# Kernel tuning notes

Hardware: AMD Instinct MI355X
Metric: run time of the kernel (lower is better)

The kernel has to match this reference:

```python
import jax, jax.numpy as jnp
import numpy as np

IN_CH = 256
OUT_CH = 256
LATENT = 512
SCALE = 1.0 / IN_CH ** 0.5


def setup_inputs() -> dict:
    key = jax.random.key(0)
    k1, k2, k3, k4 = jax.random.split(key, 4)
    return {
        "x": jax.random.normal(k1, (16, IN_CH, 64, 64), dtype=jnp.float32),
        "w": jax.random.normal(k2, (16, LATENT), dtype=jnp.float32),
        "style_w": jax.random.normal(k3, (IN_CH, LATENT), dtype=jnp.float32) * (1.0 / LATENT ** 0.5),
        "style_b": jnp.zeros((IN_CH,), dtype=jnp.float32),
        "weight": jax.random.normal(k4, (1, OUT_CH, IN_CH, 3, 3), dtype=jnp.float32),
    }


def reference(x, w, style_w, style_b, weight):
    b, c, h, ws = x.shape
    # style = Linear(latent -> in_channels), reshaped to [b,1,in,1,1]
    style = (w @ style_w.T + style_b)[:, None, :, None, None]
    wt = weight * SCALE                    # [1, O, I, 3, 3]
    wt = wt * (style + 1.0)                # [b, O, I, 3, 3]
    demod = jax.lax.rsqrt(jnp.sum(wt * wt, axis=(2, 3, 4), keepdims=True) + 1e-8)
    wt = wt * demod
    # grouped conv: fold batch into channels, groups = b
    x2 = x.reshape(1, b * c, h, ws)
    k = wt.reshape(b * OUT_CH, c, 3, 3)
    out = jax.lax.conv_general_dilated(
        x2, k,
        window_strides=(1, 1),
        padding=((1, 1), (1, 1)),
        dimension_numbers=("NCHW", "OIHW", "NCHW"),
        feature_group_count=b,
    )
    return out.reshape(b, OUT_CH, h, ws)
```

## Files before the change

### kernel.cpp

```cpp
#include <hip/hip_runtime.h>
#include <hip/hip_bf16.h>

#define IN_CH 256
#define OUT_CH 256
#define LATENT 512
#define MSCALE (1.0f / 16.0f)

typedef __attribute__((ext_vector_type(8)))  short bf16x8;
typedef __attribute__((ext_vector_type(16))) float f32x16;
typedef unsigned short u16;

__device__ __forceinline__ u16 f2bf(float f) {
  unsigned int x = __float_as_uint(f);
  x += 0x7fffu + ((x >> 16) & 1u);
  return (u16)(x >> 16);
}

__device__ __forceinline__ void gload_lds16(const u16* g, u16* l) {
#if defined(__has_builtin) && __has_builtin(__builtin_amdgcn_global_load_lds)
  __builtin_amdgcn_global_load_lds(
      (const __attribute__((address_space(1))) unsigned int*)g,
      (__attribute__((address_space(3))) unsigned int*)l, 16, 0, 0);
#else
  int lane = __builtin_amdgcn_mbcnt_hi(~0u, __builtin_amdgcn_mbcnt_lo(~0u, 0));
  ((uint4*)l)[lane] = *(const uint4*)g;
#endif
}

__global__ void k_style_demod(const float* __restrict__ w, const float* __restrict__ sw,
                              const float* __restrict__ sb, const float* __restrict__ wsq,
                              float* __restrict__ mod, float* __restrict__ demod) {
  __shared__ float ws[LATENT];
  __shared__ float m2[IN_CH];
  const int b = blockIdx.x, tid = threadIdx.x;
  ws[tid] = w[b * LATENT + tid];
  ws[tid + 256] = w[b * LATENT + 256 + tid];
  __syncthreads();
  const float4* sr = (const float4*)(sw + (size_t)tid * LATENT);
  const float4* wr = (const float4*)ws;
  float s = 0.f;
#pragma unroll 8
  for (int l = 0; l < LATENT / 4; ++l) {
    float4 a = sr[l], c = wr[l];
    s += a.x * c.x + a.y * c.y + a.z * c.z + a.w * c.w;
  }
  float m = (1.0f + s + sb[tid]) * MSCALE;
  mod[b * IN_CH + tid] = m;
  m2[tid] = m * m;
  __syncthreads();
  float acc = 1e-8f;
  const float* q = wsq + (size_t)tid * IN_CH;
#pragma unroll 4
  for (int i = 0; i < IN_CH; ++i) acc += m2[i] * q[i];
  demod[b * OUT_CH + tid] = rsqrtf(acc);
}

__global__ void k_wsq(const float* __restrict__ weight, float* __restrict__ wsq,
                      u16* __restrict__ wb) {
  const int o = blockIdx.x, i = threadIdx.x;
  const float* wp = weight + ((size_t)o * IN_CH + i) * 9;
  float s = 0.f;
#pragma unroll
  for (int t = 0; t < 9; ++t) {
    float v = wp[t];
    s += v * v;
    wb[(((size_t)t * 32 + (i >> 3)) * OUT_CH + o) * 8 + (i & 7)] = f2bf(v);
  }
  wsq[o * IN_CH + i] = s;
}

__global__ void k_pad(const float* __restrict__ x, const float* __restrict__ mod,
                      u16* __restrict__ xs) {
  const int bid = blockIdx.x;
  const int b = bid / 66, pr = bid - b * 66;
  const int tid = threadIdx.x;
  u16* rowbase = xs + (size_t)((b * 66 + pr) * 32) * 528;

  if (pr == 0 || pr == 65) {
    uint4 z = {0, 0, 0, 0};
    uint4* p = (uint4*)rowbase;
#pragma unroll
    for (int it = 0; it < 5; ++it) {
      int idx = it * 256 + tid;
      if (idx < 1056) p[idx] = z;
    }
    return;
  }

  __shared__ __align__(16) u16 lt[64][264];
  const int h = pr - 1;

#pragma unroll
  for (int it = 0; it < 16; ++it) {
    const int i = it * 16 + (tid >> 4);
    const int w4 = (tid & 15) * 4;
    float4 v = *(const float4*)(x + (((size_t)(b * IN_CH + i) * 64 + h) * 64 + w4));
    const float m = mod[b * IN_CH + i];
    lt[w4 + 0][i] = f2bf(v.x * m);
    lt[w4 + 1][i] = f2bf(v.y * m);
    lt[w4 + 2][i] = f2bf(v.z * m);
    lt[w4 + 3][i] = f2bf(v.w * m);
  }
  if (tid < 64) {
    uint4 z = {0, 0, 0, 0};
    const int G = tid & 31;
    *(uint4*)(rowbase + (size_t)G * 528 + (tid < 32 ? 0 : 65 * 8)) = z;
  }
  __syncthreads();

  const int G = tid >> 3, wlo = tid & 7;
#pragma unroll
  for (int k = 0; k < 8; ++k) {
    const int w = k * 8 + wlo;
    *(bf16x8*)(rowbase + (size_t)G * 528 + (w + 1) * 8) = *(const bf16x8*)(&lt[w][G * 8]);
  }
}

__global__ __launch_bounds__(256, 2)
void k_conv(const u16* __restrict__ xs, const u16* __restrict__ wb,
            const float* __restrict__ demod, float* __restrict__ out) {
  __shared__ __align__(16) u16 xlds[2 * 10 * 2 * 66 * 8];
  __shared__ __align__(16) u16 wlds[2 * 9 * 2 * 64 * 8];

  const int tid = threadIdx.x;
  const int lane = tid & 63;
  const int wid = tid >> 6;
  const int ol = lane & 31;
  const int hi = lane >> 5;

  const int bid = blockIdx.x;
  const int sbid = ((bid & 7) << 6) | (bid >> 3);
  const int otile = (sbid & 3) << 6;
  const int hbase = ((sbid >> 2) & 7) << 3;
  const int b = sbid >> 5;

  const u16* xsb = xs + (size_t)((b * 66 + hbase) * 32) * 528;

  int xoff[5];
#pragma unroll
  for (int it = 0; it < 5; ++it) {
    int q = it * 256 + tid;
    int r = q / 132, rem = q - r * 132;
    int g = rem / 66, c = rem - g * 66;
    xoff[it] = (r * 32 + g) * 528 + c * 8;
  }
  const int xofft = (9 * 32 + 1) * 528 + (26 + tid) * 8;
  int woff[4];
#pragma unroll
  for (int it = 0; it < 4; ++it) {
    int p = it * 256 + tid;
    int t = p >> 7, g = (p >> 6) & 1, o = p & 63;
    woff[it] = ((t * 32 + g) * OUT_CH + otile + o) * 8;
  }
  const int wofft = ((8 * 32 + ((tid >> 6) & 1)) * OUT_CH + otile + (tid & 63)) * 8;

  auto stage = [&](int buf, int ic) {
    const int ibx = ic * 1056;
    const int ibw = ic * 4096;
    u16* xd = xlds + buf * 10560;
#pragma unroll
    for (int it = 0; it < 5; ++it)
      gload_lds16(xsb + xoff[it] + ibx, xd + (size_t)(it * 256 + wid * 64) * 8);
    if (tid < 40)
      gload_lds16(xsb + xofft + ibx, xd + (size_t)(1280 + wid * 64) * 8);
    u16* wd = wlds + buf * 9216;
#pragma unroll
    for (int it = 0; it < 4; ++it)
      gload_lds16(wb + woff[it] + ibw, wd + (size_t)(it * 256 + wid * 64) * 8);
    if (tid < 128)
      gload_lds16(wb + wofft + ibw, wd + (size_t)(1024 + wid * 64) * 8);
  };

  f32x16 acc[2][4] = {};

  stage(0, 0);
  __syncthreads();

  for (int ic = 0; ic < 16; ++ic) {
    const int buf = ic & 1;
    if (ic < 15) stage(buf ^ 1, ic + 1);
    const u16* xp = xlds + buf * 10560;
    const u16* wp = wlds + buf * 9216;
    __builtin_amdgcn_s_setprio(1);
#pragma unroll
    for (int t = 0; t < 9; ++t) {
      const int dh = t / 3, dw = t - dh * 3;
      bf16x8 a0 = *(const bf16x8*)(wp + (size_t)((t * 2 + hi) * 64 + ol) * 8);
      bf16x8 a1 = *(const bf16x8*)(wp + (size_t)((t * 2 + hi) * 64 + 32 + ol) * 8);
#pragma unroll
      for (int ps = 0; ps < 4; ++ps) {
        const int r = 2 * wid + (ps >> 1) + dh;
        const int c = (ps & 1) * 32 + ol + dw;
        bf16x8 bf = *(const bf16x8*)(xp + (size_t)((r * 2 + hi) * 66 + c) * 8);
        acc[0][ps] = __builtin_amdgcn_mfma_f32_32x32x16_bf16(a0, bf, acc[0][ps], 0, 0, 0);
        acc[1][ps] = __builtin_amdgcn_mfma_f32_32x32x16_bf16(a1, bf, acc[1][ps], 0, 0, 0);
      }
    }
    __builtin_amdgcn_s_setprio(0);
    __syncthreads();
  }

  const float* dmb = demod + b * OUT_CH + otile;
  float* outb = out + (size_t)b * OUT_CH * 4096;
#pragma unroll
  for (int os = 0; os < 2; ++os) {
    float dm[16];
#pragma unroll
    for (int qd = 0; qd < 4; ++qd) {
      float4 d4 = *(const float4*)(dmb + os * 32 + qd * 8 + hi * 4);
      dm[qd * 4 + 0] = d4.x; dm[qd * 4 + 1] = d4.y;
      dm[qd * 4 + 2] = d4.z; dm[qd * 4 + 3] = d4.w;
    }
#pragma unroll
    for (int ps = 0; ps < 4; ++ps) {
      const int prow = hbase + 2 * wid + (ps >> 1);
      const int col = (ps & 1) * 32 + ol;
#pragma unroll
      for (int rr = 0; rr < 16; ++rr) {
        const int orow = (rr & 3) + 8 * (rr >> 2) + 4 * hi;
        const int o = otile + os * 32 + orow;
        outb[(size_t)o * 4096 + prow * 64 + col] = acc[os][ps][rr] * dm[rr];
      }
    }
  }
}

extern "C" void kernel_launch(void* const* d_in, const int* in_sizes, int n_in,
                              void* d_out, int out_size, void* d_ws, size_t ws_size,
                              hipStream_t stream) {
  const float* x  = (const float*)d_in[0];
  const float* w  = (const float*)d_in[1];
  const float* sw = (const float*)d_in[2];
  const float* sb = (const float*)d_in[3];
  const float* wt = (const float*)d_in[4];
  float* out = (float*)d_out;

  char* ws = (char*)d_ws;
  u16*   xs    = (u16*)(ws);
  u16*   wb    = (u16*)(ws + 35684352);
  float* mod   = (float*)(ws + 36864000);
  float* demod = (float*)(ws + 36880384);
  float* wsq   = (float*)(ws + 36896768);
  if (ws_size < 37158912u) return;

  k_wsq        <<<256, 256, 0, stream>>>(wt, wsq, wb);
  k_style_demod<<<16, 256, 0, stream>>>(w, sw, sb, wsq, mod, demod);
  k_pad        <<<16 * 66, 256, 0, stream>>>(x, mod, xs);
  k_conv       <<<512, 256, 0, stream>>>(xs, wb, demod, out);
}
```

Measured before the change: 113.4 us.

## Interleave prefetch with per-row MFMA phases and batch LDS reads ahead

```diff
diff --git a/kernel.cpp b/kernel.cpp
--- a/kernel.cpp
+++ b/kernel.cpp
@@ -154,49 +154,81 @@
   }
   const int wofft = ((8 * 32 + ((tid >> 6) & 1)) * OUT_CH + otile + (tid & 63)) * 8;
 
-  auto stage = [&](int buf, int ic) {
-    const int ibx = ic * 1056;
-    const int ibw = ic * 4096;
-    u16* xd = xlds + buf * 10560;
+  f32x16 acc[2][4] = {};
+
+  {
+    u16* xd = xlds;
+    u16* wd = wlds;
 #pragma unroll
     for (int it = 0; it < 5; ++it)
-      gload_lds16(xsb + xoff[it] + ibx, xd + (size_t)(it * 256 + wid * 64) * 8);
+      gload_lds16(xsb + xoff[it], xd + (size_t)(it * 256 + wid * 64) * 8);
     if (tid < 40)
-      gload_lds16(xsb + xofft + ibx, xd + (size_t)(1280 + wid * 64) * 8);
-    u16* wd = wlds + buf * 9216;
+      gload_lds16(xsb + xofft, xd + (size_t)(1280 + wid * 64) * 8);
 #pragma unroll
     for (int it = 0; it < 4; ++it)
-      gload_lds16(wb + woff[it] + ibw, wd + (size_t)(it * 256 + wid * 64) * 8);
+      gload_lds16(wb + woff[it], wd + (size_t)(it * 256 + wid * 64) * 8);
     if (tid < 128)
-      gload_lds16(wb + wofft + ibw, wd + (size_t)(1024 + wid * 64) * 8);
-  };
-
-  f32x16 acc[2][4] = {};
-
-  stage(0, 0);
+      gload_lds16(wb + wofft, wd + (size_t)(1024 + wid * 64) * 8);
+  }
   __syncthreads();
 
   for (int ic = 0; ic < 16; ++ic) {
     const int buf = ic & 1;
-    if (ic < 15) stage(buf ^ 1, ic + 1);
     const u16* xp = xlds + buf * 10560;
     const u16* wp = wlds + buf * 9216;
-    __builtin_amdgcn_s_setprio(1);
-#pragma unroll
-    for (int t = 0; t < 9; ++t) {
-      const int dh = t / 3, dw = t - dh * 3;
-      bf16x8 a0 = *(const bf16x8*)(wp + (size_t)((t * 2 + hi) * 64 + ol) * 8);
-      bf16x8 a1 = *(const bf16x8*)(wp + (size_t)((t * 2 + hi) * 64 + 32 + ol) * 8);
-#pragma unroll
-      for (int ps = 0; ps < 4; ++ps) {
-        const int r = 2 * wid + (ps >> 1) + dh;
-        const int c = (ps & 1) * 32 + ol + dw;
-        bf16x8 bf = *(const bf16x8*)(xp + (size_t)((r * 2 + hi) * 66 + c) * 8);
-        acc[0][ps] = __builtin_amdgcn_mfma_f32_32x32x16_bf16(a0, bf, acc[0][ps], 0, 0, 0);
-        acc[1][ps] = __builtin_amdgcn_mfma_f32_32x32x16_bf16(a1, bf, acc[1][ps], 0, 0, 0);
-      }
-    }
-    __builtin_amdgcn_s_setprio(0);
+    u16* xd = xlds + (buf ^ 1) * 10560;
+    u16* wd = wlds + (buf ^ 1) * 9216;
+    const int ibx = (ic + 1) * 1056;
+    const int ibw = (ic + 1) * 4096;
+    const bool pf = (ic < 15);
+
+#pragma unroll
+    for (int dh = 0; dh < 3; ++dh) {
+      bf16x8 A[3][2], B[4][3];
+#pragma unroll
+      for (int dw = 0; dw < 3; ++dw) {
+        const int t = dh * 3 + dw;
+        A[dw][0] = *(const bf16x8*)(wp + (size_t)((t * 2 + hi) * 64 + ol) * 8);
+        A[dw][1] = *(const bf16x8*)(wp + (size_t)((t * 2 + hi) * 64 + 32 + ol) * 8);
+#pragma unroll
+        for (int ps = 0; ps < 4; ++ps) {
+          const int r = 2 * wid + (ps >> 1) + dh;
+          const int c = (ps & 1) * 32 + ol + dw;
+          B[ps][dw] = *(const bf16x8*)(xp + (size_t)((r * 2 + hi) * 66 + c) * 8);
+        }
+      }
+      if (pf) {
+        if (dh == 0) {
+#pragma unroll
+          for (int it = 0; it < 3; ++it)
+            gload_lds16(xsb + xoff[it] + ibx, xd + (size_t)(it * 256 + wid * 64) * 8);
+        } else if (dh == 1) {
+#pragma unroll
+          for (int it = 3; it < 5; ++it)
+            gload_lds16(xsb + xoff[it] + ibx, xd + (size_t)(it * 256 + wid * 64) * 8);
+          if (tid < 40)
+            gload_lds16(xsb + xofft + ibx, xd + (size_t)(1280 + wid * 64) * 8);
+        } else {
+#pragma unroll
+          for (int it = 0; it < 4; ++it)
+            gload_lds16(wb + woff[it] + ibw, wd + (size_t)(it * 256 + wid * 64) * 8);
+          if (tid < 128)
+            gload_lds16(wb + wofft + ibw, wd + (size_t)(1024 + wid * 64) * 8);
+        }
+      }
+      __builtin_amdgcn_s_barrier();
+      __builtin_amdgcn_s_setprio(1);
+#pragma unroll
+      for (int dw = 0; dw < 3; ++dw) {
+#pragma unroll
+        for (int ps = 0; ps < 4; ++ps) {
+          acc[0][ps] = __builtin_amdgcn_mfma_f32_32x32x16_bf16(A[dw][0], B[ps][dw], acc[0][ps], 0, 0, 0);
+          acc[1][ps] = __builtin_amdgcn_mfma_f32_32x32x16_bf16(A[dw][1], B[ps][dw], acc[1][ps], 0, 0, 0);
+        }
+      }
+      __builtin_amdgcn_s_setprio(0);
+      if (dh < 2) __builtin_amdgcn_s_barrier();
+    }
     __syncthreads();
   }
 
```

New measurement: 115.8 us. 1.02x slower.
